# Kernel optimization log

Measured on AMD Instinct MI355X. Metric: run time of the kernel, lower is better.

Reference implementation:

```python
import jax, jax.numpy as jnp
import numpy as np

B, N, M, DQ, DK, DV, H = 8, 1024, 1024, 512, 512, 512, 8
DS = DV // H  # dim_split = 64
NEG = -1e38


def _ln(x, g, b, eps=1e-5):
    mu = jnp.mean(x, -1, keepdims=True)
    var = jnp.mean((x - mu) ** 2, -1, keepdims=True)
    return (x - mu) * jax.lax.rsqrt(var + eps) * g + b


def setup_inputs() -> dict:
    key = jax.random.key(0)
    ks = jax.random.split(key, 16)
    s = 0.02
    return {
        "x": jax.random.normal(ks[0], (B, N, DQ), jnp.float32),
        "y": jax.random.normal(ks[1], (B, M, DK), jnp.float32),
        "x_mask": jax.random.randint(ks[2], (B, N), 0, 2).astype(bool),
        "y_mask": jax.random.randint(ks[3], (B, M), 0, 2).astype(bool),
        "Wq": jax.random.normal(ks[4], (DQ, DV), jnp.float32) * s,
        "Wk": jax.random.normal(ks[5], (DK, DV), jnp.float32) * s,
        "Wv": jax.random.normal(ks[6], (DK, DV), jnp.float32) * s,
        "Wo": jax.random.normal(ks[7], (DV, DQ), jnp.float32) * s,
        "W1": jax.random.normal(ks[8], (DQ, DQ), jnp.float32) * s,
        "b1": jnp.zeros((DQ,), jnp.float32),
        "W2": jax.random.normal(ks[9], (DQ, DQ), jnp.float32) * s,
        "b2": jnp.zeros((DQ,), jnp.float32),
        "g1": jnp.ones((DQ,), jnp.float32),
        "be1": jnp.zeros((DQ,), jnp.float32),
        "g2": jnp.ones((DQ,), jnp.float32),
        "be2": jnp.zeros((DQ,), jnp.float32),
    }


def reference(x, y, x_mask, y_mask, Wq, Wk, Wv, Wo, W1, b1, W2, b2, g1, be1, g2, be2):
    xm = x_mask[..., None]  # [B,N,1]
    ym = y_mask[..., None]  # [B,M,1]
    x = jnp.where(xm, 0.0, x)
    y = jnp.where(ym, 0.0, y)
    # projections (no bias); masked rows stay zero, re-mask as in source
    q = jnp.where(xm, 0.0, x @ Wq).reshape(B, N, H, DS)
    k = jnp.where(ym, 0.0, y @ Wk).reshape(B, M, H, DS)
    v = jnp.where(ym, 0.0, y @ Wv).reshape(B, M, H, DS)
    # scaled dot product; NOTE: scale is sqrt(dim_v), faithful to source
    sdp = jnp.einsum('bnhd,bmhd->bhnm', q, k) / np.sqrt(DV)
    mask = x_mask[:, None, :, None] | y_mask[:, None, None, :]  # [B,1,N,M]
    sdp = jnp.where(mask, NEG, sdp)
    alpha = jax.nn.softmax(sdp, axis=-1)  # softmax over keys (slot_att=False)
    att = jnp.einsum('bhnm,bmhd->bnhd', alpha, v).reshape(B, N, DV)
    att = jnp.where(xm, 0.0, att)
    o = x + att @ Wo
    o = _ln(o, g1, be1)
    ff = jax.nn.relu(o @ W1 + b1) @ W2 + b2
    o = _ln(o + ff, g2, be2)
    return jnp.where(xm, 0.0, o)
```

## Files before the change

### kernel.cpp

```cpp
#include <hip/hip_runtime.h>
#include <hip/hip_bf16.h>

typedef __bf16 bf16;
typedef __attribute__((ext_vector_type(4))) __bf16 bf16x4;
typedef __attribute__((ext_vector_type(8))) __bf16 bf16x8;
typedef __attribute__((ext_vector_type(4))) float f32x4;

#define B_ 8
#define N_ 1024
#define M_ 1024
#define H_ 8
#define ROWS_ (B_ * N_)

__device__ __forceinline__ f32x4 mfma16(bf16x8 a, bf16x8 b, f32x4 c) {
    return __builtin_amdgcn_mfma_f32_16x16x32_bf16(a, b, c, 0, 0, 0);
}

__device__ __forceinline__ void glds16(const void* g, void* l) {
    __builtin_amdgcn_global_load_lds((const __attribute__((address_space(1))) void*)g,
                                     (__attribute__((address_space(3))) void*)l, 16, 0, 0);
}

__global__ void cvt2(const float4* __restrict__ x, const float4* __restrict__ y,
                     bf16x4* __restrict__ Xb, bf16x4* __restrict__ Yb) {
    int i = blockIdx.x * 256 + threadIdx.x;
    const float4* s;
    bf16x4* d;
    int j;
    if (i < 1048576) { s = x; d = Xb; j = i; }
    else             { s = y; d = Yb; j = i - 1048576; }
    float4 f = s[j];
    bf16x4 o = {(bf16)f.x, (bf16)f.y, (bf16)f.z, (bf16)f.w};
    d[j] = o;
}

__global__ __launch_bounds__(256) void wtrans6(const float* W0, const float* W1, const float* W2,
                                               const float* W3, const float* W4, const float* W5,
                                               bf16* T0, bf16* T1, bf16* T2, bf16* T3, bf16* T4, bf16* T5) {
    __shared__ float t[64][65];
    const float* srcs[6] = {W0, W1, W2, W3, W4, W5};
    bf16* dsts[6] = {T0, T1, T2, T3, T4, T5};
    const float* W = srcs[blockIdx.y];
    bf16* Wt = dsts[blockIdx.y];
    int k0 = (blockIdx.x >> 3) * 64, n0 = (blockIdx.x & 7) * 64;
    int tx = threadIdx.x & 63, ty = threadIdx.x >> 6;
#pragma unroll
    for (int j = 0; j < 16; ++j)
        t[ty + j * 4][tx] = W[(size_t)(k0 + ty + j * 4) * 512 + n0 + tx];
    __syncthreads();
#pragma unroll
    for (int j = 0; j < 16; ++j)
        Wt[(size_t)(n0 + ty + j * 4) * 512 + k0 + tx] = (bf16)t[tx][ty + j * 4];
}

__device__ __forceinline__ void gemm_core(const bf16* __restrict__ A, const bf16* __restrict__ Bt,
                                          int row0, int col0, bf16* As, bf16* Bs, f32x4* acc) {
    int tid = threadIdx.x, wave = tid >> 6, lane = tid & 63;
    int lr = lane & 15, q4 = lane >> 4;
    int r0 = tid >> 3, bk0 = (tid & 7) ^ (r0 & 7);
    int c1 = tid + 512, r1 = c1 >> 3, bk1 = (c1 & 7) ^ (r1 & 7);
    const bf16* Asrc0 = A + (size_t)(row0 + r0) * 512 + bk0 * 8;
    const bf16* Asrc1 = A + (size_t)(row0 + r1) * 512 + bk1 * 8;
    const bf16* Bsrc  = Bt + (size_t)(col0 + r0) * 512 + bk0 * 8;
    int wb = wave * 1024;
    for (int k0 = 0; k0 < 512; k0 += 64) {
        __syncthreads();
        glds16(Asrc0 + k0, (char*)As + wb);
        glds16(Asrc1 + k0, (char*)As + 8192 + wb);
        glds16(Bsrc + k0, (char*)Bs + wb);
        __syncthreads();
        int row = wave * 16 + lr;
        bf16x8 af0 = *(const bf16x8*)((const char*)As + (row * 8 + (q4 ^ (row & 7))) * 16);
        bf16x8 af1 = *(const bf16x8*)((const char*)As + (row * 8 + ((4 + q4) ^ (row & 7))) * 16);
#pragma unroll
        for (int ct = 0; ct < 4; ++ct) {
            int col = ct * 16 + lr;
            bf16x8 bf0 = *(const bf16x8*)((const char*)Bs + (col * 8 + (q4 ^ (col & 7))) * 16);
            bf16x8 bf1 = *(const bf16x8*)((const char*)Bs + (col * 8 + ((4 + q4) ^ (col & 7))) * 16);
            acc[ct] = mfma16(af0, bf0, acc[ct]);
            acc[ct] = mfma16(af1, bf1, acc[ct]);
        }
    }
}

__global__ __launch_bounds__(512) void proj_qkv(const bf16* __restrict__ Xb, const bf16* __restrict__ Yb,
                                                const bf16* __restrict__ Wqt, const bf16* __restrict__ Wkt,
                                                const bf16* __restrict__ Wvt,
                                                bf16* __restrict__ qb, bf16* __restrict__ kb,
                                                bf16* __restrict__ Vt) {
    __shared__ bf16 As[128 * 64];
    __shared__ bf16 Bs[64 * 64];
    int z = blockIdx.z;
    const bf16 *A, *Bt;
    int row0, col0;
    if (z == 0)      { A = Xb;  Bt = Wqt; row0 = blockIdx.x * 128; col0 = blockIdx.y * 64; }
    else if (z == 1) { A = Yb;  Bt = Wkt; row0 = blockIdx.x * 128; col0 = blockIdx.y * 64; }
    else { A = Wvt; Bt = Yb; int flat = blockIdx.y * 64 + blockIdx.x; row0 = (flat & 3) * 128; col0 = (flat >> 2) * 64; }
    const f32x4 z4 = {0.f, 0.f, 0.f, 0.f};
    f32x4 acc[4] = {z4, z4, z4, z4};
    gemm_core(A, Bt, row0, col0, As, Bs, acc);
    int wave = threadIdx.x >> 6, lane = threadIdx.x & 63, lr = lane & 15, q4 = lane >> 4;
    bf16* dst = (z == 0) ? qb : kb;
#pragma unroll
    for (int ct = 0; ct < 4; ++ct) {
        int col = col0 + ct * 16 + lr;
#pragma unroll
        for (int r = 0; r < 4; ++r) {
            int row = row0 + wave * 16 + q4 * 4 + r;
            bf16 v = (bf16)acc[ct][r];
            if (z < 2) dst[(size_t)row * 512 + col] = v;
            else Vt[(size_t)((col >> 10) * 512 + row) * 1024 + (col & 1023)] = v;
        }
    }
}

template <int MODE>
__global__ __launch_bounds__(512) void gemm_bt(const bf16* __restrict__ A, const bf16* __restrict__ Bt,
                                               const float* __restrict__ bias, void* __restrict__ Cout) {
    __shared__ bf16 As[128 * 64];
    __shared__ bf16 Bs[64 * 64];
    int row0 = blockIdx.x * 128, col0 = blockIdx.y * 64;
    const f32x4 z4 = {0.f, 0.f, 0.f, 0.f};
    f32x4 acc[4] = {z4, z4, z4, z4};
    gemm_core(A, Bt, row0, col0, As, Bs, acc);
    int wave = threadIdx.x >> 6, lane = threadIdx.x & 63, lr = lane & 15, q4 = lane >> 4;
#pragma unroll
    for (int ct = 0; ct < 4; ++ct) {
        int col = col0 + ct * 16 + lr;
        float bv = (MODE >= 2) ? bias[col] : 0.0f;
#pragma unroll
        for (int r = 0; r < 4; ++r) {
            int row = row0 + wave * 16 + q4 * 4 + r;
            float v = acc[ct][r] + bv;
            if (MODE == 3) v = fmaxf(v, 0.0f);
            if (MODE == 3) ((bf16*)Cout)[(size_t)row * 512 + col] = (bf16)v;
            else           ((float*)Cout)[(size_t)row * 512 + col] = v;
        }
    }
}

__global__ __launch_bounds__(512) void attn(const bf16* __restrict__ Q, const bf16* __restrict__ Kb,
                                            const bf16* __restrict__ Vt, const int* __restrict__ ymask,
                                            bf16* __restrict__ att) {
    __shared__ bf16 Ks[64 * 64];
    __shared__ bf16 Vs[64 * 64];
    __shared__ bf16 Ps[8][16 * 72];

    int bid = blockIdx.x;
    int bh = bid & 63, n0 = (bid >> 6) * 128;
    int b = bh >> 3, h = bh & 7;
    int tid = threadIdx.x, wave = tid >> 6, lane = tid & 63;
    int lr = lane & 15, q4 = lane >> 4;
    const float scale = 0.044194173824159216f;

    const bf16* qp = Q + (size_t)((b << 10) + n0 + wave * 16 + lr) * 512 + h * 64 + q4 * 8;
    bf16x8 aq0 = *(const bf16x8*)qp;
    bf16x8 aq1 = *(const bf16x8*)(qp + 32);

    int r = tid >> 3, bk = (tid & 7) ^ (r & 7);
    const bf16* Ksrc = Kb + (size_t)((b << 10) + r) * 512 + h * 64 + bk * 8;
    const bf16* Vsrc = Vt + (size_t)(b * 512 + h * 64 + r) * 1024 + bk * 8;
    int wb = wave * 1024;

    const f32x4 zv = {0.f, 0.f, 0.f, 0.f};
    f32x4 O[4] = {zv, zv, zv, zv};
    float lsum[4] = {0.f, 0.f, 0.f, 0.f};

    for (int m0 = 0; m0 < M_; m0 += 64) {
        int mk = ymask[(b << 10) + m0 + lane];
        __syncthreads();
        glds16(Ksrc + (size_t)m0 * 512, (char*)Ks + wb);
        glds16(Vsrc + m0, (char*)Vs + wb);
        __syncthreads();

#pragma unroll
        for (int nt = 0; nt < 4; ++nt) {
            int krow = nt * 16 + lr;
            bf16x8 kf0 = *(const bf16x8*)((const char*)Ks + (krow * 8 + (q4 ^ (krow & 7))) * 16);
            bf16x8 kf1 = *(const bf16x8*)((const char*)Ks + (krow * 8 + ((4 + q4) ^ (krow & 7))) * 16);
            int mkv = __shfl(mk, krow);
            f32x4 s = mfma16(aq0, kf0, zv);
            s = mfma16(aq1, kf1, s);
#pragma unroll
            for (int rr = 0; rr < 4; ++rr) {
                float p = mkv ? 0.0f : __expf(s[rr] * scale);
                lsum[rr] += p;
                Ps[wave][(q4 * 4 + rr) * 72 + krow] = (bf16)p;
            }
        }
        bf16x8 ap0 = *(const bf16x8*)&Ps[wave][lr * 72 + q4 * 8];
        bf16x8 ap1 = *(const bf16x8*)&Ps[wave][lr * 72 + 32 + q4 * 8];
#pragma unroll
        for (int dt = 0; dt < 4; ++dt) {
            int vrow = dt * 16 + lr;
            bf16x8 vf0 = *(const bf16x8*)((const char*)Vs + (vrow * 8 + (q4 ^ (vrow & 7))) * 16);
            bf16x8 vf1 = *(const bf16x8*)((const char*)Vs + (vrow * 8 + ((4 + q4) ^ (vrow & 7))) * 16);
            O[dt] = mfma16(ap0, vf0, O[dt]);
            O[dt] = mfma16(ap1, vf1, O[dt]);
        }
    }

#pragma unroll
    for (int rr = 0; rr < 4; ++rr) {
        float v = lsum[rr];
        v += __shfl_xor(v, 1); v += __shfl_xor(v, 2);
        v += __shfl_xor(v, 4); v += __shfl_xor(v, 8);
        lsum[rr] = (v > 0.0f) ? (1.0f / v) : 0.0f;
    }
#pragma unroll
    for (int dt = 0; dt < 4; ++dt)
#pragma unroll
        for (int rr = 0; rr < 4; ++rr) {
            int row = n0 + wave * 16 + q4 * 4 + rr;
            att[(size_t)((b << 10) + row) * 512 + h * 64 + dt * 16 + lr] =
                (bf16)(O[dt][rr] * lsum[rr]);
        }
}

__global__ __launch_bounds__(256) void ln1_k(const float* __restrict__ X, const float* __restrict__ R,
                                             const float* __restrict__ g, const float* __restrict__ be,
                                             float* __restrict__ O, bf16* __restrict__ Obf) {
    int row = blockIdx.x, t = threadIdx.x;
    size_t base = (size_t)row * 512;
    float t0 = X[base + t] + R[base + t];
    float t1 = X[base + 256 + t] + R[base + 256 + t];
    float s = t0 + t1, sq = t0 * t0 + t1 * t1;
#pragma unroll
    for (int off = 1; off < 64; off <<= 1) { s += __shfl_xor(s, off); sq += __shfl_xor(sq, off); }
    __shared__ float ls[4], lq[4];
    int w = t >> 6;
    if ((t & 63) == 0) { ls[w] = s; lq[w] = sq; }
    __syncthreads();
    s = ls[0] + ls[1] + ls[2] + ls[3];
    sq = lq[0] + lq[1] + lq[2] + lq[3];
    float mu = s * (1.0f / 512.0f);
    float var = sq * (1.0f / 512.0f) - mu * mu;
    float rs = rsqrtf(var + 1e-5f);
    float o0 = (t0 - mu) * rs * g[t] + be[t];
    float o1 = (t1 - mu) * rs * g[256 + t] + be[256 + t];
    O[base + t] = o0; O[base + 256 + t] = o1;
    Obf[base + t] = (bf16)o0; Obf[base + 256 + t] = (bf16)o1;
}

__global__ __launch_bounds__(256) void ln2_k(const float* __restrict__ O, const float* __restrict__ F,
                                             const float* __restrict__ g, const float* __restrict__ be,
                                             const int* __restrict__ xmask, float* __restrict__ out) {
    int row = blockIdx.x, t = threadIdx.x;
    size_t base = (size_t)row * 512;
    float t0 = O[base + t] + F[base + t];
    float t1 = O[base + 256 + t] + F[base + 256 + t];
    float s = t0 + t1, sq = t0 * t0 + t1 * t1;
#pragma unroll
    for (int off = 1; off < 64; off <<= 1) { s += __shfl_xor(s, off); sq += __shfl_xor(sq, off); }
    __shared__ float ls[4], lq[4];
    int w = t >> 6;
    if ((t & 63) == 0) { ls[w] = s; lq[w] = sq; }
    __syncthreads();
    s = ls[0] + ls[1] + ls[2] + ls[3];
    sq = lq[0] + lq[1] + lq[2] + lq[3];
    float mu = s * (1.0f / 512.0f);
    float var = sq * (1.0f / 512.0f) - mu * mu;
    float rs = rsqrtf(var + 1e-5f);
    int msk = xmask[row];
    float o0 = (t0 - mu) * rs * g[t] + be[t];
    float o1 = (t1 - mu) * rs * g[256 + t] + be[256 + t];
    out[base + t] = msk ? 0.0f : o0;
    out[base + 256 + t] = msk ? 0.0f : o1;
}

extern "C" void kernel_launch(void* const* d_in, const int* in_sizes, int n_in,
                              void* d_out, int out_size, void* d_ws, size_t ws_size,
                              hipStream_t stream) {
    const float* x   = (const float*)d_in[0];
    const float* y   = (const float*)d_in[1];
    const int*   xm  = (const int*)d_in[2];
    const int*   ym  = (const int*)d_in[3];
    const float* Wq  = (const float*)d_in[4];
    const float* Wk  = (const float*)d_in[5];
    const float* Wv  = (const float*)d_in[6];
    const float* Wo  = (const float*)d_in[7];
    const float* W1  = (const float*)d_in[8];
    const float* b1  = (const float*)d_in[9];
    const float* W2  = (const float*)d_in[10];
    const float* b2  = (const float*)d_in[11];
    const float* g1  = (const float*)d_in[12];
    const float* be1 = (const float*)d_in[13];
    const float* g2  = (const float*)d_in[14];
    const float* be2 = (const float*)d_in[15];

    char* ws = (char*)d_ws;
    const size_t WT_SZ  = 512 * 512 * sizeof(bf16);
    const size_t XB_SZ  = (size_t)ROWS_ * 512 * sizeof(bf16);
    const size_t F32_SZ = (size_t)ROWS_ * 512 * sizeof(float);

    bf16* Wqt = (bf16*)(ws + 0 * WT_SZ);
    bf16* Wkt = (bf16*)(ws + 1 * WT_SZ);
    bf16* Wvt = (bf16*)(ws + 2 * WT_SZ);
    bf16* Wot = (bf16*)(ws + 3 * WT_SZ);
    bf16* W1t = (bf16*)(ws + 4 * WT_SZ);
    bf16* W2t = (bf16*)(ws + 5 * WT_SZ);
    size_t off = 6 * WT_SZ;
    bf16* Xb  = (bf16*)(ws + off); off += XB_SZ;
    bf16* Yb  = (bf16*)(ws + off); off += XB_SZ;
    bf16* qb  = (bf16*)(ws + off); off += XB_SZ;
    bf16* kb  = (bf16*)(ws + off); off += XB_SZ;
    bf16* Vt  = (bf16*)(ws + off); off += XB_SZ;
    float* awo = (float*)(ws + off); off += F32_SZ;
    float* ob  = (float*)(ws + off); off += F32_SZ;
    bf16* attb = Xb;
    bf16* obf  = qb;
    bf16* hb   = Yb;
    float* fb  = awo;

    cvt2<<<8192, 256, 0, stream>>>((const float4*)x, (const float4*)y, (bf16x4*)Xb, (bf16x4*)Yb);
    wtrans6<<<dim3(64, 6), 256, 0, stream>>>(Wq, Wk, Wv, Wo, W1, W2,
                                             Wqt, Wkt, Wvt, Wot, W1t, W2t);

    proj_qkv<<<dim3(64, 8, 3), 512, 0, stream>>>(Xb, Yb, Wqt, Wkt, Wvt, qb, kb, Vt);

    attn<<<512, 512, 0, stream>>>(qb, kb, Vt, ym, attb);

    dim3 gg(64, 8);
    gemm_bt<0><<<gg, 512, 0, stream>>>(attb, Wot, nullptr, awo);
    ln1_k<<<ROWS_, 256, 0, stream>>>(x, awo, g1, be1, ob, obf);
    gemm_bt<3><<<gg, 512, 0, stream>>>(obf, W1t, b1, hb);
    gemm_bt<2><<<gg, 512, 0, stream>>>(hb, W2t, b2, fb);
    ln2_k<<<ROWS_, 256, 0, stream>>>(ob, fb, g2, be2, xm, (float*)d_out);
}
```

Measured before the change: 224.9 us.

## Merge prep kernels, use 4-wave GEMM blocks with 2x2 tiles, widen attention KV step

Three changes. The bf16 conversion and weight-transpose kernels are merged into one launch to cut launch overhead. GEMM blocks drop from 512 to 256 threads, so each wave now computes 32 rows and reuses its B fragments across two row tiles, which lowers LDS traffic per MFMA but raises register use. The attention kernel now loads 128 keys per barrier pair instead of 64, halving the number of synchronizations at the cost of doubled K/V shared memory.

```diff
diff --git a/kernel.cpp b/kernel.cpp
--- a/kernel.cpp
+++ b/kernel.cpp
@@ -21,28 +21,32 @@
                                      (__attribute__((address_space(3))) void*)l, 16, 0, 0);
 }
 
-__global__ void cvt2(const float4* __restrict__ x, const float4* __restrict__ y,
-                     bf16x4* __restrict__ Xb, bf16x4* __restrict__ Yb) {
-    int i = blockIdx.x * 256 + threadIdx.x;
-    const float4* s;
-    bf16x4* d;
-    int j;
-    if (i < 1048576) { s = x; d = Xb; j = i; }
-    else             { s = y; d = Yb; j = i - 1048576; }
-    float4 f = s[j];
-    bf16x4 o = {(bf16)f.x, (bf16)f.y, (bf16)f.z, (bf16)f.w};
-    d[j] = o;
-}
-
-__global__ __launch_bounds__(256) void wtrans6(const float* W0, const float* W1, const float* W2,
-                                               const float* W3, const float* W4, const float* W5,
-                                               bf16* T0, bf16* T1, bf16* T2, bf16* T3, bf16* T4, bf16* T5) {
+__global__ __launch_bounds__(256) void prep(const float* __restrict__ x, const float* __restrict__ y,
+                                            bf16* __restrict__ Xb, bf16* __restrict__ Yb,
+                                            const float* W0, const float* W1, const float* W2,
+                                            const float* W3, const float* W4, const float* W5,
+                                            bf16* T0, bf16* T1, bf16* T2, bf16* T3, bf16* T4, bf16* T5) {
     __shared__ float t[64][65];
+    int bid = blockIdx.x;
+    if (bid < 8192) {
+        int i = bid * 256 + threadIdx.x;
+        const float4* s;
+        bf16x4* d;
+        int j;
+        if (i < 1048576) { s = (const float4*)x; d = (bf16x4*)Xb; j = i; }
+        else             { s = (const float4*)y; d = (bf16x4*)Yb; j = i - 1048576; }
+        float4 f = s[j];
+        bf16x4 o = {(bf16)f.x, (bf16)f.y, (bf16)f.z, (bf16)f.w};
+        d[j] = o;
+        return;
+    }
+    int wb = bid - 8192;
     const float* srcs[6] = {W0, W1, W2, W3, W4, W5};
     bf16* dsts[6] = {T0, T1, T2, T3, T4, T5};
-    const float* W = srcs[blockIdx.y];
-    bf16* Wt = dsts[blockIdx.y];
-    int k0 = (blockIdx.x >> 3) * 64, n0 = (blockIdx.x & 7) * 64;
+    const float* W = srcs[wb >> 6];
+    bf16* Wt = dsts[wb >> 6];
+    int tile = wb & 63;
+    int k0 = (tile >> 3) * 64, n0 = (tile & 7) * 64;
     int tx = threadIdx.x & 63, ty = threadIdx.x >> 6;
 #pragma unroll
     for (int j = 0; j < 16; ++j)
@@ -54,36 +58,55 @@
 }
 
 __device__ __forceinline__ void gemm_core(const bf16* __restrict__ A, const bf16* __restrict__ Bt,
-                                          int row0, int col0, bf16* As, bf16* Bs, f32x4* acc) {
+                                          int row0, int col0, bf16* As, bf16* Bs, f32x4 acc[2][4]) {
     int tid = threadIdx.x, wave = tid >> 6, lane = tid & 63;
     int lr = lane & 15, q4 = lane >> 4;
-    int r0 = tid >> 3, bk0 = (tid & 7) ^ (r0 & 7);
-    int c1 = tid + 512, r1 = c1 >> 3, bk1 = (c1 & 7) ^ (r1 & 7);
-    const bf16* Asrc0 = A + (size_t)(row0 + r0) * 512 + bk0 * 8;
-    const bf16* Asrc1 = A + (size_t)(row0 + r1) * 512 + bk1 * 8;
-    const bf16* Bsrc  = Bt + (size_t)(col0 + r0) * 512 + bk0 * 8;
+    const bf16* Asrc[4];
+    const bf16* Bsrc[2];
+#pragma unroll
+    for (int s = 0; s < 4; ++s) {
+        int c = tid + s * 256, r = c >> 3, bk = (c & 7) ^ (r & 7);
+        Asrc[s] = A + (size_t)(row0 + r) * 512 + bk * 8;
+    }
+#pragma unroll
+    for (int s = 0; s < 2; ++s) {
+        int c = tid + s * 256, r = c >> 3, bk = (c & 7) ^ (r & 7);
+        Bsrc[s] = Bt + (size_t)(col0 + r) * 512 + bk * 8;
+    }
     int wb = wave * 1024;
     for (int k0 = 0; k0 < 512; k0 += 64) {
         __syncthreads();
-        glds16(Asrc0 + k0, (char*)As + wb);
-        glds16(Asrc1 + k0, (char*)As + 8192 + wb);
-        glds16(Bsrc + k0, (char*)Bs + wb);
+#pragma unroll
+        for (int s = 0; s < 4; ++s) glds16(Asrc[s] + k0, (char*)As + s * 4096 + wb);
+#pragma unroll
+        for (int s = 0; s < 2; ++s) glds16(Bsrc[s] + k0, (char*)Bs + s * 4096 + wb);
         __syncthreads();
-        int row = wave * 16 + lr;
-        bf16x8 af0 = *(const bf16x8*)((const char*)As + (row * 8 + (q4 ^ (row & 7))) * 16);
-        bf16x8 af1 = *(const bf16x8*)((const char*)As + (row * 8 + ((4 + q4) ^ (row & 7))) * 16);
+        bf16x8 af[2][2], bfr[4][2];
+#pragma unroll
+        for (int rt = 0; rt < 2; ++rt) {
+            int row = wave * 32 + rt * 16 + lr;
+#pragma unroll
+            for (int c = 0; c < 2; ++c)
+                af[rt][c] = *(const bf16x8*)((const char*)As + (row * 8 + ((c * 4 + q4) ^ (row & 7))) * 16);
+        }
 #pragma unroll
         for (int ct = 0; ct < 4; ++ct) {
             int col = ct * 16 + lr;
-            bf16x8 bf0 = *(const bf16x8*)((const char*)Bs + (col * 8 + (q4 ^ (col & 7))) * 16);
-            bf16x8 bf1 = *(const bf16x8*)((const char*)Bs + (col * 8 + ((4 + q4) ^ (col & 7))) * 16);
-            acc[ct] = mfma16(af0, bf0, acc[ct]);
-            acc[ct] = mfma16(af1, bf1, acc[ct]);
-        }
-    }
-}
-
-__global__ __launch_bounds__(512) void proj_qkv(const bf16* __restrict__ Xb, const bf16* __restrict__ Yb,
+#pragma unroll
+            for (int c = 0; c < 2; ++c)
+                bfr[ct][c] = *(const bf16x8*)((const char*)Bs + (col * 8 + ((c * 4 + q4) ^ (col & 7))) * 16);
+        }
+#pragma unroll
+        for (int rt = 0; rt < 2; ++rt)
+#pragma unroll
+            for (int ct = 0; ct < 4; ++ct) {
+                acc[rt][ct] = mfma16(af[rt][0], bfr[ct][0], acc[rt][ct]);
+                acc[rt][ct] = mfma16(af[rt][1], bfr[ct][1], acc[rt][ct]);
+            }
+    }
+}
+
+__global__ __launch_bounds__(256) void proj_qkv(const bf16* __restrict__ Xb, const bf16* __restrict__ Yb,
                                                 const bf16* __restrict__ Wqt, const bf16* __restrict__ Wkt,
                                                 const bf16* __restrict__ Wvt,
                                                 bf16* __restrict__ qb, bf16* __restrict__ kb,
@@ -97,53 +120,57 @@
     else if (z == 1) { A = Yb;  Bt = Wkt; row0 = blockIdx.x * 128; col0 = blockIdx.y * 64; }
     else { A = Wvt; Bt = Yb; int flat = blockIdx.y * 64 + blockIdx.x; row0 = (flat & 3) * 128; col0 = (flat >> 2) * 64; }
     const f32x4 z4 = {0.f, 0.f, 0.f, 0.f};
-    f32x4 acc[4] = {z4, z4, z4, z4};
+    f32x4 acc[2][4] = {{z4, z4, z4, z4}, {z4, z4, z4, z4}};
     gemm_core(A, Bt, row0, col0, As, Bs, acc);
     int wave = threadIdx.x >> 6, lane = threadIdx.x & 63, lr = lane & 15, q4 = lane >> 4;
     bf16* dst = (z == 0) ? qb : kb;
 #pragma unroll
-    for (int ct = 0; ct < 4; ++ct) {
-        int col = col0 + ct * 16 + lr;
-#pragma unroll
-        for (int r = 0; r < 4; ++r) {
-            int row = row0 + wave * 16 + q4 * 4 + r;
-            bf16 v = (bf16)acc[ct][r];
-            if (z < 2) dst[(size_t)row * 512 + col] = v;
-            else Vt[(size_t)((col >> 10) * 512 + row) * 1024 + (col & 1023)] = v;
-        }
-    }
+    for (int rt = 0; rt < 2; ++rt)
+#pragma unroll
+        for (int ct = 0; ct < 4; ++ct) {
+            int col = col0 + ct * 16 + lr;
+#pragma unroll
+            for (int r = 0; r < 4; ++r) {
+                int row = row0 + wave * 32 + rt * 16 + q4 * 4 + r;
+                bf16 v = (bf16)acc[rt][ct][r];
+                if (z < 2) dst[(size_t)row * 512 + col] = v;
+                else Vt[(size_t)((col >> 10) * 512 + row) * 1024 + (col & 1023)] = v;
+            }
+        }
 }
 
 template <int MODE>
-__global__ __launch_bounds__(512) void gemm_bt(const bf16* __restrict__ A, const bf16* __restrict__ Bt,
+__global__ __launch_bounds__(256) void gemm_bt(const bf16* __restrict__ A, const bf16* __restrict__ Bt,
                                                const float* __restrict__ bias, void* __restrict__ Cout) {
     __shared__ bf16 As[128 * 64];
     __shared__ bf16 Bs[64 * 64];
     int row0 = blockIdx.x * 128, col0 = blockIdx.y * 64;
     const f32x4 z4 = {0.f, 0.f, 0.f, 0.f};
-    f32x4 acc[4] = {z4, z4, z4, z4};
+    f32x4 acc[2][4] = {{z4, z4, z4, z4}, {z4, z4, z4, z4}};
     gemm_core(A, Bt, row0, col0, As, Bs, acc);
     int wave = threadIdx.x >> 6, lane = threadIdx.x & 63, lr = lane & 15, q4 = lane >> 4;
 #pragma unroll
-    for (int ct = 0; ct < 4; ++ct) {
-        int col = col0 + ct * 16 + lr;
-        float bv = (MODE >= 2) ? bias[col] : 0.0f;
-#pragma unroll
-        for (int r = 0; r < 4; ++r) {
-            int row = row0 + wave * 16 + q4 * 4 + r;
-            float v = acc[ct][r] + bv;
-            if (MODE == 3) v = fmaxf(v, 0.0f);
-            if (MODE == 3) ((bf16*)Cout)[(size_t)row * 512 + col] = (bf16)v;
-            else           ((float*)Cout)[(size_t)row * 512 + col] = v;
-        }
-    }
+    for (int rt = 0; rt < 2; ++rt)
+#pragma unroll
+        for (int ct = 0; ct < 4; ++ct) {
+            int col = col0 + ct * 16 + lr;
+            float bv = (MODE >= 2) ? bias[col] : 0.0f;
+#pragma unroll
+            for (int r = 0; r < 4; ++r) {
+                int row = row0 + wave * 32 + rt * 16 + q4 * 4 + r;
+                float v = acc[rt][ct][r] + bv;
+                if (MODE == 3) v = fmaxf(v, 0.0f);
+                if (MODE == 3) ((bf16*)Cout)[(size_t)row * 512 + col] = (bf16)v;
+                else           ((float*)Cout)[(size_t)row * 512 + col] = v;
+            }
+        }
 }
 
 __global__ __launch_bounds__(512) void attn(const bf16* __restrict__ Q, const bf16* __restrict__ Kb,
                                             const bf16* __restrict__ Vt, const int* __restrict__ ymask,
                                             bf16* __restrict__ att) {
-    __shared__ bf16 Ks[64 * 64];
-    __shared__ bf16 Vs[64 * 64];
+    __shared__ bf16 Ks[2][64 * 64];
+    __shared__ bf16 Vs[2][64 * 64];
     __shared__ bf16 Ps[8][16 * 72];
 
     int bid = blockIdx.x;
@@ -166,37 +193,46 @@
     f32x4 O[4] = {zv, zv, zv, zv};
     float lsum[4] = {0.f, 0.f, 0.f, 0.f};
 
-    for (int m0 = 0; m0 < M_; m0 += 64) {
-        int mk = ymask[(b << 10) + m0 + lane];
+    for (int m0 = 0; m0 < M_; m0 += 128) {
+        int mk0 = ymask[(b << 10) + m0 + lane];
+        int mk1 = ymask[(b << 10) + m0 + 64 + lane];
         __syncthreads();
-        glds16(Ksrc + (size_t)m0 * 512, (char*)Ks + wb);
-        glds16(Vsrc + m0, (char*)Vs + wb);
+        glds16(Ksrc + (size_t)m0 * 512, (char*)Ks[0] + wb);
+        glds16(Ksrc + (size_t)(m0 + 64) * 512, (char*)Ks[1] + wb);
+        glds16(Vsrc + m0, (char*)Vs[0] + wb);
+        glds16(Vsrc + m0 + 64, (char*)Vs[1] + wb);
         __syncthreads();
 
 #pragma unroll
-        for (int nt = 0; nt < 4; ++nt) {
-            int krow = nt * 16 + lr;
-            bf16x8 kf0 = *(const bf16x8*)((const char*)Ks + (krow * 8 + (q4 ^ (krow & 7))) * 16);
-            bf16x8 kf1 = *(const bf16x8*)((const char*)Ks + (krow * 8 + ((4 + q4) ^ (krow & 7))) * 16);
-            int mkv = __shfl(mk, krow);
-            f32x4 s = mfma16(aq0, kf0, zv);
-            s = mfma16(aq1, kf1, s);
-#pragma unroll
-            for (int rr = 0; rr < 4; ++rr) {
-                float p = mkv ? 0.0f : __expf(s[rr] * scale);
-                lsum[rr] += p;
-                Ps[wave][(q4 * 4 + rr) * 72 + krow] = (bf16)p;
-            }
-        }
-        bf16x8 ap0 = *(const bf16x8*)&Ps[wave][lr * 72 + q4 * 8];
-        bf16x8 ap1 = *(const bf16x8*)&Ps[wave][lr * 72 + 32 + q4 * 8];
-#pragma unroll
-        for (int dt = 0; dt < 4; ++dt) {
-            int vrow = dt * 16 + lr;
-            bf16x8 vf0 = *(const bf16x8*)((const char*)Vs + (vrow * 8 + (q4 ^ (vrow & 7))) * 16);
-            bf16x8 vf1 = *(const bf16x8*)((const char*)Vs + (vrow * 8 + ((4 + q4) ^ (vrow & 7))) * 16);
-            O[dt] = mfma16(ap0, vf0, O[dt]);
-            O[dt] = mfma16(ap1, vf1, O[dt]);
+        for (int half = 0; half < 2; ++half) {
+            const char* K_ = (const char*)Ks[half];
+            const char* V_ = (const char*)Vs[half];
+            int mkh = half ? mk1 : mk0;
+#pragma unroll
+            for (int nt = 0; nt < 4; ++nt) {
+                int krow = nt * 16 + lr;
+                bf16x8 kf0 = *(const bf16x8*)(K_ + (krow * 8 + (q4 ^ (krow & 7))) * 16);
+                bf16x8 kf1 = *(const bf16x8*)(K_ + (krow * 8 + ((4 + q4) ^ (krow & 7))) * 16);
+                int mkv = __shfl(mkh, krow);
+                f32x4 s = mfma16(aq0, kf0, zv);
+                s = mfma16(aq1, kf1, s);
+#pragma unroll
+                for (int rr = 0; rr < 4; ++rr) {
+                    float p = mkv ? 0.0f : __expf(s[rr] * scale);
+                    lsum[rr] += p;
+                    Ps[wave][(q4 * 4 + rr) * 72 + krow] = (bf16)p;
+                }
+            }
+            bf16x8 ap0 = *(const bf16x8*)&Ps[wave][lr * 72 + q4 * 8];
+            bf16x8 ap1 = *(const bf16x8*)&Ps[wave][lr * 72 + 32 + q4 * 8];
+#pragma unroll
+            for (int dt = 0; dt < 4; ++dt) {
+                int vrow = dt * 16 + lr;
+                bf16x8 vf0 = *(const bf16x8*)(V_ + (vrow * 8 + (q4 ^ (vrow & 7))) * 16);
+                bf16x8 vf1 = *(const bf16x8*)(V_ + (vrow * 8 + ((4 + q4) ^ (vrow & 7))) * 16);
+                O[dt] = mfma16(ap0, vf0, O[dt]);
+                O[dt] = mfma16(ap1, vf1, O[dt]);
+            }
         }
     }
 
@@ -312,18 +348,17 @@
     bf16* hb   = Yb;
     float* fb  = awo;
 
-    cvt2<<<8192, 256, 0, stream>>>((const float4*)x, (const float4*)y, (bf16x4*)Xb, (bf16x4*)Yb);
-    wtrans6<<<dim3(64, 6), 256, 0, stream>>>(Wq, Wk, Wv, Wo, W1, W2,
-                                             Wqt, Wkt, Wvt, Wot, W1t, W2t);
-
-    proj_qkv<<<dim3(64, 8, 3), 512, 0, stream>>>(Xb, Yb, Wqt, Wkt, Wvt, qb, kb, Vt);
+    prep<<<8576, 256, 0, stream>>>(x, y, Xb, Yb, Wq, Wk, Wv, Wo, W1, W2,
+                                   Wqt, Wkt, Wvt, Wot, W1t, W2t);
+
+    proj_qkv<<<dim3(64, 8, 3), 256, 0, stream>>>(Xb, Yb, Wqt, Wkt, Wvt, qb, kb, Vt);
 
     attn<<<512, 512, 0, stream>>>(qb, kb, Vt, ym, attb);
 
     dim3 gg(64, 8);
-    gemm_bt<0><<<gg, 512, 0, stream>>>(attb, Wot, nullptr, awo);
+    gemm_bt<0><<<gg, 256, 0, stream>>>(attb, Wot, nullptr, awo);
     ln1_k<<<ROWS_, 256, 0, stream>>>(x, awo, g1, be1, ob, obf);
-    gemm_bt<3><<<gg, 512, 0, stream>>>(obf, W1t, b1, hb);
-    gemm_bt<2><<<gg, 512, 0, stream>>>(hb, W2t, b2, fb);
+    gemm_bt<3><<<gg, 256, 0, stream>>>(obf, W1t, b1, hb);
+    gemm_bt<2><<<gg, 256, 0, stream>>>(hb, W2t, b2, fb);
     ln2_k<<<ROWS_, 256, 0, stream>>>(ob, fb, g2, be2, xm, (float*)d_out);
 }
```

Result: faster. 218.2 us (-3.0%).
